# Optimization experiments

Hardware: AMD Instinct MI355X
Metric: run time of the kernel (lower is better)

## Reference

```python
import jax, jax.numpy as jnp
import numpy as np

SCALE = 0.17677669529663687  # 1/sqrt(head_dim=32)
EPS = 1e-12

def setup_inputs() -> dict:
    key = jax.random.key(0)
    k1, k2 = jax.random.split(key)
    B, H, HW, KK, D = 4, 8, 4096, 9, 32
    logits = jax.random.normal(k1, (B, H, HW, KK, KK), dtype=jnp.float32)
    v = jax.random.normal(k2, (B, H, HW, KK, D), dtype=jnp.float32)
    return {"logits": logits, "v": v}

def reference(logits, v):
    # logits: [B,heads,HW,KK,KK], v: [B,heads,HW,KK,head_dim]
    B, H, HW, KK, _ = logits.shape
    D = v.shape[-1]
    x = logits * SCALE
    x = x - jnp.max(x, axis=-1, keepdims=True)
    e = jnp.exp(x)
    probs = e / (jnp.sum(e, axis=-1, keepdims=True) + EPS)
    # out[b,h,hw,i,d] = sum_j probs[b,h,hw,i,j] * v[b,h,hw,j,d]
    out = jnp.einsum('bnwij,bnwjd->bnwid', probs, v)
    # flatten: out_flat[b, (h*D + d)*KK + i, hw]
    out_flat = jnp.transpose(out, (0, 1, 4, 3, 2)).reshape(B, H * D * KK, HW)
    return out_flat
```

## Files before the change

### kernel.cpp

```cpp
#include <hip/hip_runtime.h>

#define HW_DIM 4096
#define NHW 32
#define NT 512
#define NCHUNK (HW_DIM / NHW)


__global__ __launch_bounds__(NT)
void attn9_kernel(const float* __restrict__ logits,
                  const float* __restrict__ v,
                  float* __restrict__ out)
{
    __shared__ float v_s[NHW * 288];
    __shared__ float lp_s[NHW * 81];

    const int t = threadIdx.x;
    const int bid = blockIdx.x;
    const int chunk = bid & (NCHUNK - 1);
    const int bh = bid >> 7;

    const int hw0 = bh * HW_DIM + chunk * NHW;

    {
        const float4* vg = reinterpret_cast<const float4*>(v + (size_t)hw0 * 288);
        float4* vs4 = reinterpret_cast<float4*>(v_s);
        #pragma unroll
        for (int k = 0; k < 5; ++k) {
            int idx4 = t + k * NT;
            if (idx4 < (NHW * 288) / 4) {
                float4 val = vg[idx4];
                int hwl = idx4 / 72;
                int q   = idx4 - hwl * 72;
                vs4[hwl * 72 + (q ^ (hwl & 7))] = val;
            }
        }
    }

    {
        const float4* lg4 = reinterpret_cast<const float4*>(logits + (size_t)hw0 * 81);
        float4* ls4 = reinterpret_cast<float4*>(lp_s);
        #pragma unroll
        for (int k = 0; k < 2; ++k) {
            int idx4 = t + k * NT;
            if (idx4 < (NHW * 81) / 4) ls4[idx4] = lg4[idx4];
        }
    }

    __syncthreads();

    if (t < NHW * 9) {
        const int hwl = t / 9;
        const int i = t - hwl * 9;
        float* row = &lp_s[hwl * 81 + i * 9];
        float x[9];
        #pragma unroll
        for (int j = 0; j < 9; ++j) x[j] = row[j] * 0.17677669529663687f;
        float m = x[0];
        #pragma unroll
        for (int j = 1; j < 9; ++j) m = fmaxf(m, x[j]);
        float e[9];
        float s = 0.f;
        #pragma unroll
        for (int j = 0; j < 9; ++j) { e[j] = expf(x[j] - m); s += e[j]; }
        const float inv = 1.0f / (s + 1e-12f);
        #pragma unroll
        for (int j = 0; j < 9; ++j) row[j] = e[j] * inv;
    }

    __syncthreads();

    const int hw = t & (NHW - 1);
    const int dg = t >> 5;
    const int d0 = dg * 2;

    const float2* vp = reinterpret_cast<const float2*>(
        reinterpret_cast<const char*>(v_s)
        + (size_t)hw * 1152
        + (((d0 >> 2) ^ (hw & 7)) << 4)
        + ((d0 & 3) << 2));
    float va[9], vb[9];
    #pragma unroll
    for (int j = 0; j < 9; ++j) {
        float2 vv = vp[j * 16];
        va[j] = vv.x; vb[j] = vv.y;
    }

    float* ob = out + (size_t)bh * 288 * HW_DIM + chunk * NHW + hw;
    const float* prow = &lp_s[hw * 81];
    #pragma unroll
    for (int i = 0; i < 9; ++i) {
        float a0 = 0.f, a1 = 0.f;
        #pragma unroll
        for (int j = 0; j < 9; ++j) {
            float p = prow[i * 9 + j];
            a0 = fmaf(p, va[j], a0);
            a1 = fmaf(p, vb[j], a1);
        }
        ob[(size_t)(d0 * 9 + i) * HW_DIM]       = a0;
        ob[(size_t)((d0 + 1) * 9 + i) * HW_DIM] = a1;
    }
}

extern "C" void kernel_launch(void* const* d_in, const int* in_sizes, int n_in,
                              void* d_out, int out_size, void* d_ws, size_t ws_size,
                              hipStream_t stream) {
    const float* logits = (const float*)d_in[0];
    const float* v      = (const float*)d_in[1];
    float* out          = (float*)d_out;
    const int grid = 4 * 8 * NCHUNK;
    attn9_kernel<<<grid, NT, 0, stream>>>(logits, v, out);
}
```

Before: 287.6 us.

## Double block size and stage V loads in registers to overlap with softmax

Each block now covers 64 HW positions with 1024 threads, and shared memory moves to a dynamic allocation of about 94 KB. V tiles are loaded into registers before the softmax and written to shared memory only after it, so the global V load latency can overlap the softmax computation. The output mapping changes so each 64-lane wave covers contiguous HW positions, giving 256-byte coalesced stores. The larger blocks and extra registers may reduce occupancy and halve the grid size.

```diff
diff --git a/kernel.cpp b/kernel.cpp
--- a/kernel.cpp
+++ b/kernel.cpp
@@ -1,9 +1,11 @@
 #include <hip/hip_runtime.h>
 
 #define HW_DIM 4096
-#define NHW 32
-#define NT 512
+#define NHW 64
+#define NT 1024
 #define NCHUNK (HW_DIM / NHW)
+#define V_F4 (NHW * 72)
+#define SMEM_BYTES (V_F4 * 16 + NHW * 81 * 4)
 
 
 __global__ __launch_bounds__(NT)
@@ -11,47 +13,36 @@
                   const float* __restrict__ v,
                   float* __restrict__ out)
 {
-    __shared__ float v_s[NHW * 288];
-    __shared__ float lp_s[NHW * 81];
+    extern __shared__ char smem[];
+    float4* vs4 = reinterpret_cast<float4*>(smem);
+    float*  lp  = reinterpret_cast<float*>(smem + V_F4 * 16);
 
     const int t = threadIdx.x;
     const int bid = blockIdx.x;
     const int chunk = bid & (NCHUNK - 1);
-    const int bh = bid >> 7;
-
+    const int bh = bid >> 6;
     const int hw0 = bh * HW_DIM + chunk * NHW;
 
-    {
-        const float4* vg = reinterpret_cast<const float4*>(v + (size_t)hw0 * 288);
-        float4* vs4 = reinterpret_cast<float4*>(v_s);
-        #pragma unroll
-        for (int k = 0; k < 5; ++k) {
-            int idx4 = t + k * NT;
-            if (idx4 < (NHW * 288) / 4) {
-                float4 val = vg[idx4];
-                int hwl = idx4 / 72;
-                int q   = idx4 - hwl * 72;
-                vs4[hwl * 72 + (q ^ (hwl & 7))] = val;
-            }
-        }
-    }
+    const float4* vg = reinterpret_cast<const float4*>(v + (size_t)hw0 * 288);
+    float4 vr0 = vg[t];
+    float4 vr1 = vg[t + NT];
+    float4 vr2 = vg[t + 2 * NT];
+    float4 vr3 = vg[t + 3 * NT];
+    float4 vr4 = {0.f, 0.f, 0.f, 0.f};
+    if (t < V_F4 - 4 * NT) vr4 = vg[t + 4 * NT];
 
     {
         const float4* lg4 = reinterpret_cast<const float4*>(logits + (size_t)hw0 * 81);
-        float4* ls4 = reinterpret_cast<float4*>(lp_s);
-        #pragma unroll
-        for (int k = 0; k < 2; ++k) {
-            int idx4 = t + k * NT;
-            if (idx4 < (NHW * 81) / 4) ls4[idx4] = lg4[idx4];
-        }
+        float4* lp4 = reinterpret_cast<float4*>(lp);
+        lp4[t] = lg4[t];
+        if (t < NHW * 81 / 4 - NT) lp4[t + NT] = lg4[t + NT];
     }
-
     __syncthreads();
 
     if (t < NHW * 9) {
         const int hwl = t / 9;
         const int i = t - hwl * 9;
-        float* row = &lp_s[hwl * 81 + i * 9];
+        float* row = &lp[hwl * 81 + i * 9];
         float x[9];
         #pragma unroll
         for (int j = 0; j < 9; ++j) x[j] = row[j] * 0.17677669529663687f;
@@ -67,26 +58,38 @@
         for (int j = 0; j < 9; ++j) row[j] = e[j] * inv;
     }
 
+    {
+        #pragma unroll
+        for (int k = 0; k < 5; ++k) {
+            int idx4 = t + k * NT;
+            if (k < 4 || t < V_F4 - 4 * NT) {
+                int hwl = idx4 / 72;
+                int q   = idx4 - hwl * 72;
+                float4 val = (k == 0) ? vr0 : (k == 1) ? vr1 : (k == 2) ? vr2
+                           : (k == 3) ? vr3 : vr4;
+                vs4[hwl * 72 + (q ^ (hwl & 7))] = val;
+            }
+        }
+    }
     __syncthreads();
 
     const int hw = t & (NHW - 1);
-    const int dg = t >> 5;
+    const int dg = t >> 6;
     const int d0 = dg * 2;
 
-    const float2* vp = reinterpret_cast<const float2*>(
-        reinterpret_cast<const char*>(v_s)
+    const char* vbase = reinterpret_cast<const char*>(vs4)
         + (size_t)hw * 1152
         + (((d0 >> 2) ^ (hw & 7)) << 4)
-        + ((d0 & 3) << 2));
+        + ((d0 & 3) << 2);
     float va[9], vb[9];
     #pragma unroll
     for (int j = 0; j < 9; ++j) {
-        float2 vv = vp[j * 16];
+        float2 vv = *reinterpret_cast<const float2*>(vbase + j * 128);
         va[j] = vv.x; vb[j] = vv.y;
     }
 
     float* ob = out + (size_t)bh * 288 * HW_DIM + chunk * NHW + hw;
-    const float* prow = &lp_s[hw * 81];
+    const float* prow = &lp[hw * 81];
     #pragma unroll
     for (int i = 0; i < 9; ++i) {
         float a0 = 0.f, a1 = 0.f;
@@ -107,6 +110,8 @@
     const float* logits = (const float*)d_in[0];
     const float* v      = (const float*)d_in[1];
     float* out          = (float*)d_out;
+    hipFuncSetAttribute(reinterpret_cast<const void*>(attn9_kernel),
+                        hipFuncAttributeMaxDynamicSharedMemorySize, SMEM_BYTES);
     const int grid = 4 * 8 * NCHUNK;
-    attn9_kernel<<<grid, NT, 0, stream>>>(logits, v, out);
+    attn9_kernel<<<grid, NT, SMEM_BYTES, stream>>>(logits, v, out);
 }
```

After: 293.7 us. 1.02x slower.
